# Kernel tuning notes

Measured on AMD Instinct MI355X. Metric: run time of the kernel, lower is better.

Reference implementation:

```python
import jax, jax.numpy as jnp
import numpy as np

G = 20000   # total_genes = nodes per graph = output dim
HID = 64    # hidden_channels
H = 4       # attention heads (concat=False -> mean over heads)
E = 640000  # edges (avg degree 32)
B = 128     # batch of cell-line samples
PD = 600    # perturbation feature dim
NEG_SLOPE = 0.2


def _gat(x, edge_index, W, a_src, a_dst, b, heads):
    """PyG GATConv with add_self_loops=True, concat=False (head mean)."""
    N = x.shape[0]
    C = W.shape[1] // heads
    h = (x @ W).reshape(N, heads, C)              # [N,H,C]
    loop = jnp.arange(N, dtype=edge_index.dtype)
    src = jnp.concatenate([edge_index[0], loop])  # [E+N]
    dst = jnp.concatenate([edge_index[1], loop])
    e_src = jnp.sum(h * a_src[None], axis=-1)     # [N,H]
    e_dst = jnp.sum(h * a_dst[None], axis=-1)
    e = jax.nn.leaky_relu(e_src[src] + e_dst[dst], NEG_SLOPE)  # [E+N,H]
    # segment softmax over incoming edges of each target node
    m = jax.ops.segment_max(e, dst, num_segments=N)
    ex = jnp.exp(e - m[dst])
    denom = jax.ops.segment_sum(ex, dst, num_segments=N)
    alpha = ex / denom[dst]                        # [E+N,H]
    out = jax.ops.segment_sum(h[src] * alpha[:, :, None], dst, num_segments=N)
    return out.mean(axis=1) + b                    # concat=False -> mean heads


def _mlp(x, W1, b1, W2, b2):
    # MLP([a,b,c], 'Sigmoid'): Linear -> Sigmoid -> Linear (last act dropped)
    return jax.nn.sigmoid(x @ W1 + b1) @ W2 + b2


def setup_inputs() -> dict:
    key = jax.random.key(0)
    ks = jax.random.split(key, 26)
    s = 0.05  # small init to keep sigmoids in their active range
    rn = lambda k, shp: jax.random.normal(k, shp, jnp.float32)
    return {
        "x": rn(ks[0], (G, 1)),
        "edge_index": jax.random.randint(ks[1], (2, E), 0, G, dtype=jnp.int32),
        "pos": jnp.arange(G, dtype=jnp.int32),
        "ctrl": rn(ks[2], (B, G)),
        "pert": rn(ks[3], (B, PD)),
        "gene_embed": rn(ks[4], (G, HID)) * s,
        "conv1_W": rn(ks[5], (1 + HID, H * HID)) * s,
        "conv1_as": rn(ks[6], (H, HID)) * s,
        "conv1_ad": rn(ks[7], (H, HID)) * s,
        "conv1_b": rn(ks[8], (HID,)) * s,
        "lin1_W": rn(ks[9], (1 + HID, HID)) * s,
        "lin1_b": rn(ks[10], (HID,)) * s,
        "conv2_W": rn(ks[11], (HID, H * 1)) * s,
        "conv2_as": rn(ks[12], (H, 1)) * s,
        "conv2_ad": rn(ks[13], (H, 1)) * s,
        "conv2_b": rn(ks[14], (1,)) * s,
        "lin2_W": rn(ks[15], (HID, 1)) * s,
        "lin2_b": rn(ks[16], (1,)) * s,
        "pert_W1": rn(ks[17], (PD, 128)) * s,
        "pert_b1": rn(ks[18], (128,)) * s,
        "pert_W2": rn(ks[19], (128, HID)) * s,
        "pert_b2": rn(ks[20], (HID,)) * s,
        "pred_W1": rn(ks[21], (G + HID, 1024)) * s,
        "pred_b1": rn(ks[22], (1024,)) * s,
        "pred_W2": rn(ks[23], (1024, G)) * s,
        "pred_b2": rn(ks[24], (G,)) * s,
    }


def reference(x, edge_index, pos, ctrl, pert, gene_embed,
              conv1_W, conv1_as, conv1_ad, conv1_b, lin1_W, lin1_b,
              conv2_W, conv2_as, conv2_ad, conv2_b, lin2_W, lin2_b,
              pert_W1, pert_b1, pert_W2, pert_b2,
              pred_W1, pred_b1, pred_W2, pred_b2):
    # per-graph GNN (single cell-type key), all_feat=True
    xc = jnp.concatenate([x, gene_embed[pos]], axis=1)         # [G, 1+HID]
    h1 = jax.nn.sigmoid(_gat(xc, edge_index, conv1_W, conv1_as, conv1_ad, conv1_b, H)
                        + xc @ lin1_W + lin1_b)                # [G, HID]
    h2 = jax.nn.sigmoid(_gat(h1, edge_index, conv2_W, conv2_as, conv2_ad, conv2_b, H)
                        + h1 @ lin2_W + lin2_b)                # [G, 1]
    feat = h2[:, 0]                                            # dense batch squeeze -> [G]
    # every sample in the batch uses this cell type's features
    z = feat[None, :] + ctrl                                   # [B, G]
    p = _mlp(pert, pert_W1, pert_b1, pert_W2, pert_b2)         # embd_pert -> [B, HID]
    inp = jnp.concatenate([z, p], axis=1)                      # [B, G+HID]
    return _mlp(inp, pred_W1, pred_b1, pred_W2, pred_b2)       # [B, G]
```

## Files before the change

### kernel.cpp

```cpp
#include <hip/hip_runtime.h>
#include <math.h>

#define G 20000
#define E_EDGES 640000
#define HID 64
#define NHEAD 4
#define BATCH 128
#define PD 600
#define NEG 0.2f
#define MAXE 256

#define KA1 20096
#define NSTEP1 628
#define KSPLIT1 32
#define KA2 1024

#define ROWS_HC 16

typedef float v4f __attribute__((ext_vector_type(4)));
typedef short short8 __attribute__((ext_vector_type(8)));

__device__ __forceinline__ float sigmoidf_(float x){ return 1.0f/(1.0f+__expf(-x)); }
__device__ __forceinline__ float leakyf_(float x){ return x>=0.f ? x : NEG*x; }
__device__ __forceinline__ unsigned short f2bf(float f){
    unsigned int u = __float_as_uint(f);
    return (unsigned short)((u + 0x7FFFu + ((u >> 16) & 1u)) >> 16);
}
__device__ __forceinline__ float bf2f(unsigned short b){
    return __uint_as_float(((unsigned int)b) << 16);
}

__global__ __launch_bounds__(320)
void k_hc(const float* __restrict__ x, const int* __restrict__ pos,
          const float* __restrict__ ge, const float* __restrict__ Wc,
          const float* __restrict__ Wl, const float* __restrict__ as_,
          const float* __restrict__ ad_,
          unsigned short* __restrict__ hcb, float* __restrict__ hlin,
          float* __restrict__ es, float* __restrict__ ed)
{
    int t = threadIdx.x;
    int rb = blockIdx.x * ROWS_HC;
    __shared__ float xc[ROWS_HC][68];
    for (int l = t; l < ROWS_HC*65; l += 320){
        int r = l / 65, k = l - r*65;
        int row = rb + r;
        float v = 0.f;
        if (row < G) v = (k == 0) ? x[row] : ge[pos[row]*HID + (k-1)];
        xc[r][k] = v;
    }
    float wcol[65];
    if (t < 256){
        #pragma unroll
        for (int k = 0; k < 65; ++k) wcol[k] = Wc[k*256 + t];
    } else {
        int c = t - 256;
        #pragma unroll
        for (int k = 0; k < 65; ++k) wcol[k] = Wl[k*64 + c];
    }
    float a_s = 0.f, a_d = 0.f;
    if (t < 256){ a_s = as_[t]; a_d = ad_[t]; }
    __syncthreads();

    int nrow = G - rb; if (nrow > ROWS_HC) nrow = ROWS_HC;
    for (int r = 0; r < nrow; ++r){
        int row = rb + r;
        const float4* xr = (const float4*)&xc[r][0];
        float acc = 0.f;
        #pragma unroll
        for (int k4 = 0; k4 < 16; ++k4){
            float4 v = xr[k4];
            acc += v.x*wcol[4*k4] + v.y*wcol[4*k4+1] + v.z*wcol[4*k4+2] + v.w*wcol[4*k4+3];
        }
        acc += xc[r][64] * wcol[64];
        if (t < 256){
            hcb[(size_t)row*256 + t] = f2bf(acc);
            float v1 = acc * a_s, v2 = acc * a_d;
            #pragma unroll
            for (int m = 32; m; m >>= 1){ v1 += __shfl_xor(v1, m); v2 += __shfl_xor(v2, m); }
            if ((t & 63) == 0){ int h = t >> 6; es[row*4+h] = v1; ed[row*4+h] = v2; }
        } else {
            hlin[(size_t)row*64 + (t - 256)] = acc;
        }
    }
}

__global__ void k_hist(const int* __restrict__ ei, int* __restrict__ cnt){
    int e = blockIdx.x*blockDim.x + threadIdx.x;
    if (e < E_EDGES) atomicAdd(&cnt[ei[E_EDGES + e]], 1);
}
__global__ void k_scan(const int* __restrict__ cnt, int* __restrict__ offs,
                       int* __restrict__ cur)
{
    __shared__ int ts[1024];
    int t = threadIdx.x;
    int base = t * 20;
    int loc[20];
    int s = 0;
    #pragma unroll
    for (int j = 0; j < 20; ++j){
        int i = base + j;
        int v = (i < G) ? cnt[i] : 0;
        loc[j] = s; s += v;
    }
    ts[t] = s;
    __syncthreads();
    for (int off = 1; off < 1024; off <<= 1){
        int add = (t >= off) ? ts[t - off] : 0;
        __syncthreads();
        ts[t] += add;
        __syncthreads();
    }
    int tb = (t == 0) ? 0 : ts[t - 1];
    #pragma unroll
    for (int j = 0; j < 20; ++j){
        int i = base + j;
        if (i < G){ int o = tb + loc[j]; offs[i] = o; cur[i] = o; }
    }
    if (t == 0) offs[G] = ts[1023];
}
__global__ void k_scatter(const int* __restrict__ ei, int* __restrict__ cur, int* __restrict__ csr){
    int e = blockIdx.x*blockDim.x + threadIdx.x;
    if (e < E_EDGES){
        int d = ei[E_EDGES + e];
        int p = atomicAdd(&cur[d], 1);
        csr[p] = ei[e];
    }
}

__global__ __launch_bounds__(256)
void k_gat1(const unsigned short* __restrict__ hcb, const float* __restrict__ hlin,
            const float* __restrict__ es, const float* __restrict__ ed,
            const int* __restrict__ offs, const int* __restrict__ csr,
            const float* __restrict__ bc1, const float* __restrict__ bl1,
            float* __restrict__ h1)
{
    int d = blockIdx.x; int t = threadIdx.x;
    int lane = t & 63, wv = t >> 6;
    __shared__ float4 cache[MAXE];
    __shared__ int    ssrc[MAXE];
    __shared__ float  wredm[4][4];
    __shared__ float  wreds[4][4];
    __shared__ float  red[256];
    int o = offs[d];
    int deg = offs[d+1] - o;
    int total = deg + 1;
    if (total > MAXE) total = MAXE;
    float4 edv = *(const float4*)(ed + d*4);
    float mx0=-1e30f, mx1=-1e30f, mx2=-1e30f, mx3=-1e30f;
    for (int idx = t; idx < total; idx += 256){
        int s = (idx < deg) ? csr[o + idx] : d;
        ssrc[idx] = s;
        float4 ev = *(const float4*)(es + s*4);
        float e0 = leakyf_(ev.x + edv.x);
        float e1 = leakyf_(ev.y + edv.y);
        float e2 = leakyf_(ev.z + edv.z);
        float e3 = leakyf_(ev.w + edv.w);
        cache[idx] = make_float4(e0, e1, e2, e3);
        mx0 = fmaxf(mx0, e0); mx1 = fmaxf(mx1, e1);
        mx2 = fmaxf(mx2, e2); mx3 = fmaxf(mx3, e3);
    }
    #pragma unroll
    for (int m = 32; m; m >>= 1){
        mx0 = fmaxf(mx0, __shfl_xor(mx0, m)); mx1 = fmaxf(mx1, __shfl_xor(mx1, m));
        mx2 = fmaxf(mx2, __shfl_xor(mx2, m)); mx3 = fmaxf(mx3, __shfl_xor(mx3, m));
    }
    if (lane == 0){ wredm[wv][0]=mx0; wredm[wv][1]=mx1; wredm[wv][2]=mx2; wredm[wv][3]=mx3; }
    __syncthreads();
    float m0 = fmaxf(fmaxf(wredm[0][0], wredm[1][0]), fmaxf(wredm[2][0], wredm[3][0]));
    float m1 = fmaxf(fmaxf(wredm[0][1], wredm[1][1]), fmaxf(wredm[2][1], wredm[3][1]));
    float m2 = fmaxf(fmaxf(wredm[0][2], wredm[1][2]), fmaxf(wredm[2][2], wredm[3][2]));
    float m3 = fmaxf(fmaxf(wredm[0][3], wredm[1][3]), fmaxf(wredm[2][3], wredm[3][3]));
    float s0=0.f, s1=0.f, s2=0.f, s3=0.f;
    for (int idx = t; idx < total; idx += 256){
        float4 cv = cache[idx];
        float e0 = __expf(cv.x - m0);
        float e1 = __expf(cv.y - m1);
        float e2 = __expf(cv.z - m2);
        float e3 = __expf(cv.w - m3);
        cache[idx] = make_float4(e0, e1, e2, e3);
        s0 += e0; s1 += e1; s2 += e2; s3 += e3;
    }
    #pragma unroll
    for (int m = 32; m; m >>= 1){
        s0 += __shfl_xor(s0, m); s1 += __shfl_xor(s1, m);
        s2 += __shfl_xor(s2, m); s3 += __shfl_xor(s3, m);
    }
    if (lane == 0){ wreds[wv][0]=s0; wreds[wv][1]=s1; wreds[wv][2]=s2; wreds[wv][3]=s3; }
    __syncthreads();
    float inv = 1.0f / (wreds[0][wv] + wreds[1][wv] + wreds[2][wv] + wreds[3][wv]);
    float acc0 = 0.f, acc1 = 0.f;
    int idx = 0;
    for (; idx + 2 <= total; idx += 2){
        int sA = ssrc[idx], sB = ssrc[idx+1];
        float aA = ((const float*)&cache[idx])[wv];
        float aB = ((const float*)&cache[idx+1])[wv];
        acc0 += aA * bf2f(hcb[(size_t)sA*256 + t]);
        acc1 += aB * bf2f(hcb[(size_t)sB*256 + t]);
    }
    if (idx < total){
        acc0 += ((const float*)&cache[idx])[wv] * bf2f(hcb[(size_t)ssrc[idx]*256 + t]);
    }
    red[t] = (acc0 + acc1) * inv;
    __syncthreads();
    if (t < 64){
        float sum = red[t] + red[64+t] + red[128+t] + red[192+t];
        float val = 0.25f*sum + bc1[t] + hlin[(size_t)d*64 + t] + bl1[t];
        h1[d*64 + t] = sigmoidf_(val);
    }
}

__global__ void k_conv2prep(const float* __restrict__ h1, const float* __restrict__ W2c,
                            const float* __restrict__ as2, const float* __restrict__ ad2,
                            const float* __restrict__ Wl2, float* __restrict__ hh2,
                            float* __restrict__ es2, float* __restrict__ ed2,
                            float* __restrict__ lv)
{
    int i = blockIdx.x; int k = threadIdx.x;
    float hv = h1[i*64 + k];
    #pragma unroll
    for (int j = 0; j < 4; ++j){
        float v = hv * W2c[k*4 + j];
        for (int m = 32; m; m >>= 1) v += __shfl_xor(v, m);
        if (k == 0){ hh2[i*4+j] = v; es2[i*4+j] = v*as2[j]; ed2[i*4+j] = v*ad2[j]; }
    }
    float v = hv * Wl2[k];
    for (int m = 32; m; m >>= 1) v += __shfl_xor(v, m);
    if (k == 0) lv[i] = v;
}

__global__ void k_gat2(const float* __restrict__ hh2, const float* __restrict__ es2,
                       const float* __restrict__ ed2, const int* __restrict__ offs,
                       const int* __restrict__ csr, const float* __restrict__ lv,
                       const float* __restrict__ bc2, const float* __restrict__ bl2,
                       float* __restrict__ feat)
{
    int d = blockIdx.x; int j = threadIdx.x;
    int o = offs[d];
    int deg = offs[d+1] - o;
    int total = deg + 1;
    float edst[4];
    #pragma unroll
    for (int h = 0; h < 4; ++h) edst[h] = ed2[d*4+h];
    float lmax[4] = {-1e30f,-1e30f,-1e30f,-1e30f};
    for (int idx = j; idx < total; idx += 64){
        int s = (idx < deg) ? csr[o + idx] : d;
        #pragma unroll
        for (int h = 0; h < 4; ++h)
            lmax[h] = fmaxf(lmax[h], leakyf_(es2[s*4+h] + edst[h]));
    }
    #pragma unroll
    for (int h = 0; h < 4; ++h)
        for (int m = 32; m; m >>= 1) lmax[h] = fmaxf(lmax[h], __shfl_xor(lmax[h], m));
    float lsum[4] = {0.f,0.f,0.f,0.f};
    float lnum[4] = {0.f,0.f,0.f,0.f};
    for (int idx = j; idx < total; idx += 64){
        int s = (idx < deg) ? csr[o + idx] : d;
        #pragma unroll
        for (int h = 0; h < 4; ++h){
            float e  = leakyf_(es2[s*4+h] + edst[h]);
            float ex = __expf(e - lmax[h]);
            lsum[h] += ex;
            lnum[h] += ex * hh2[s*4+h];
        }
    }
    #pragma unroll
    for (int h = 0; h < 4; ++h){
        for (int m = 32; m; m >>= 1){ lsum[h] += __shfl_xor(lsum[h], m); lnum[h] += __shfl_xor(lnum[h], m); }
    }
    if (j == 0){
        float sum = 0.f;
        #pragma unroll
        for (int h = 0; h < 4; ++h) sum += lnum[h] / lsum[h];
        feat[d] = sigmoidf_(0.25f*sum + bc2[0] + lv[d] + bl2[0]);
    }
}

__global__ void k_prepA(const float* __restrict__ ctrl, const float* __restrict__ feat,
                        unsigned short* __restrict__ Abf)
{
    int col = blockIdx.x*256 + threadIdx.x;
    int row = blockIdx.y;
    if (col < 20000)
        Abf[(size_t)row*KA1 + col] = f2bf(ctrl[(size_t)row*20000 + col] + feat[col]);
}

__global__ void k_pert(const float* __restrict__ pert, const float* __restrict__ W1,
                       const float* __restrict__ b1, const float* __restrict__ W2,
                       const float* __restrict__ b2, unsigned short* __restrict__ Abf)
{
    int r = blockIdx.x; int t = threadIdx.x;
    __shared__ float hid[128];
    float acc = 0.f;
    for (int k = 0; k < PD; ++k) acc += pert[r*PD + k] * W1[k*128 + t];
    hid[t] = sigmoidf_(acc + b1[t]);
    __syncthreads();
    if (t < 64){
        float a2 = 0.f;
        for (int k = 0; k < 128; ++k) a2 += hid[k] * W2[k*64 + t];
        Abf[(size_t)r*KA1 + 20000 + t] = f2bf(a2 + b2[t]);
    } else if (t < 96){
        Abf[(size_t)r*KA1 + 20000 + t] = 0;
    }
}

__global__ __launch_bounds__(256, 2)
void k_gemm1m(const unsigned short* __restrict__ Abf, const float* __restrict__ W1,
              float* __restrict__ part)
{
    int t = threadIdx.x;
    int lane = t & 63, wv = t >> 6;
    int lane16 = lane & 15, quad = lane >> 4, quad8 = quad * 8;
    int colbase = blockIdx.x * 64;
    int ks = blockIdx.y;
    int sbeg = (ks * NSTEP1) / KSPLIT1;
    int send = ((ks + 1) * NSTEP1) / KSPLIT1;
    int nsteps = send - sbeg;
    int kbeg = sbeg * 32;
    __shared__ unsigned short Bs[2][32*64];

    v4f acc[8];
    #pragma unroll
    for (int i = 0; i < 8; ++i) acc[i] = (v4f){0.f,0.f,0.f,0.f};

    int krow = t >> 3;
    int ng   = (t & 7) * 8;
    {
        int kg = kbeg + krow;
        short8 p;
        if (kg < 20064){
            float4 a = *(const float4*)(W1 + (size_t)kg*1024 + colbase + ng);
            float4 b = *(const float4*)(W1 + (size_t)kg*1024 + colbase + ng + 4);
            p[0]=(short)f2bf(a.x); p[1]=(short)f2bf(a.y); p[2]=(short)f2bf(a.z); p[3]=(short)f2bf(a.w);
            p[4]=(short)f2bf(b.x); p[5]=(short)f2bf(b.y); p[6]=(short)f2bf(b.z); p[7]=(short)f2bf(b.w);
        } else {
            p = (short8){0,0,0,0,0,0,0,0};
        }
        *(short8*)&Bs[0][krow*64 + ng] = p;
    }
    __syncthreads();

    int cur = 0;
    for (int s = 0; s < nsteps; ++s){
        int kg = kbeg + s*32;
        short8 bfrag;
        #pragma unroll
        for (int j = 0; j < 8; ++j)
            bfrag[j] = (short)Bs[cur][(quad8 + j)*64 + wv*16 + lane16];
        float w[8];
        bool more = (s + 1) < nsteps;
        if (more){
            int kn = kg + 32 + krow;
            if (kn < 20064){
                float4 a = *(const float4*)(W1 + (size_t)kn*1024 + colbase + ng);
                float4 b = *(const float4*)(W1 + (size_t)kn*1024 + colbase + ng + 4);
                w[0]=a.x; w[1]=a.y; w[2]=a.z; w[3]=a.w; w[4]=b.x; w[5]=b.y; w[6]=b.z; w[7]=b.w;
            } else {
                #pragma unroll
                for (int i = 0; i < 8; ++i) w[i] = 0.f;
            }
        }
        #pragma unroll
        for (int mt = 0; mt < 8; ++mt){
            short8 af = *(const short8*)(Abf + (size_t)(mt*16 + lane16)*KA1 + kg + quad8);
            acc[mt] = __builtin_amdgcn_mfma_f32_16x16x32_bf16(af, bfrag, acc[mt], 0, 0, 0);
        }
        if (more){
            short8 p;
            #pragma unroll
            for (int i = 0; i < 8; ++i) p[i] = (short)f2bf(w[i]);
            *(short8*)&Bs[cur^1][krow*64 + ng] = p;
        }
        __syncthreads();
        cur ^= 1;
    }
    float* dst = part + (size_t)ks * 131072;
    int col = colbase + wv*16 + lane16;
    #pragma unroll
    for (int mt = 0; mt < 8; ++mt)
        #pragma unroll
        for (int r = 0; r < 4; ++r)
            dst[(size_t)(mt*16 + quad*4 + r)*1024 + col] = acc[mt][r];
}

__global__ void k_reduce(const float* __restrict__ part, const float* __restrict__ b1,
                         unsigned short* __restrict__ hidbf)
{
    int row = blockIdx.x;
    int col = blockIdx.y*256 + threadIdx.x;
    float s = 0.f;
    #pragma unroll
    for (int ks = 0; ks < KSPLIT1; ++ks)
        s += part[(size_t)ks*131072 + (size_t)row*1024 + col];
    hidbf[(size_t)row*1024 + col] = f2bf(sigmoidf_(s + b1[col]));
}

__global__ __launch_bounds__(256, 2)
void k_gemm2m(const unsigned short* __restrict__ hidbf, const float* __restrict__ W2,
              const float* __restrict__ b2, float* __restrict__ out)
{
    int t = threadIdx.x;
    int lane = t & 63, wv = t >> 6;
    int lane16 = lane & 15, quad = lane >> 4, quad8 = quad * 8;
    int colbase = blockIdx.x * 64;
    int rbase   = blockIdx.y * 64;
    __shared__ unsigned short Bs[2][32*64];

    v4f acc[4];
    #pragma unroll
    for (int i = 0; i < 4; ++i) acc[i] = (v4f){0.f,0.f,0.f,0.f};

    int krow = t >> 3;
    int ng   = (t & 7) * 8;
    bool cv = (colbase + ng) < 20000;
    {
        short8 p = (short8){0,0,0,0,0,0,0,0};
        if (cv){
            float4 a = *(const float4*)(W2 + (size_t)krow*20000 + colbase + ng);
            float4 b = *(const float4*)(W2 + (size_t)krow*20000 + colbase + ng + 4);
            p[0]=(short)f2bf(a.x); p[1]=(short)f2bf(a.y); p[2]=(short)f2bf(a.z); p[3]=(short)f2bf(a.w);
            p[4]=(short)f2bf(b.x); p[5]=(short)f2bf(b.y); p[6]=(short)f2bf(b.z); p[7]=(short)f2bf(b.w);
        }
        *(short8*)&Bs[0][krow*64 + ng] = p;
    }
    __syncthreads();

    int cur = 0;
    for (int s = 0; s < 32; ++s){
        int kg = s*32;
        short8 bfrag;
        #pragma unroll
        for (int j = 0; j < 8; ++j)
            bfrag[j] = (short)Bs[cur][(quad8 + j)*64 + wv*16 + lane16];
        float w[8];
        bool more = s < 31;
        if (more){
            if (cv){
                int kn = kg + 32 + krow;
                float4 a = *(const float4*)(W2 + (size_t)kn*20000 + colbase + ng);
                float4 b = *(const float4*)(W2 + (size_t)kn*20000 + colbase + ng + 4);
                w[0]=a.x; w[1]=a.y; w[2]=a.z; w[3]=a.w; w[4]=b.x; w[5]=b.y; w[6]=b.z; w[7]=b.w;
            } else {
                #pragma unroll
                for (int i = 0; i < 8; ++i) w[i] = 0.f;
            }
        }
        #pragma unroll
        for (int mt = 0; mt < 4; ++mt){
            short8 af = *(const short8*)(hidbf + (size_t)(rbase + mt*16 + lane16)*KA2 + kg + quad8);
            acc[mt] = __builtin_amdgcn_mfma_f32_16x16x32_bf16(af, bfrag, acc[mt], 0, 0, 0);
        }
        if (more){
            short8 p;
            #pragma unroll
            for (int i = 0; i < 8; ++i) p[i] = (short)f2bf(w[i]);
            *(short8*)&Bs[cur^1][krow*64 + ng] = p;
        }
        __syncthreads();
        cur ^= 1;
    }
    int col = colbase + wv*16 + lane16;
    if (col < 20000){
        float bb = b2[col];
        #pragma unroll
        for (int mt = 0; mt < 4; ++mt)
            #pragma unroll
            for (int r = 0; r < 4; ++r)
                out[(size_t)(rbase + mt*16 + quad*4 + r)*20000 + col] = acc[mt][r] + bb;
    }
}

extern "C" void kernel_launch(void* const* d_in, const int* in_sizes, int n_in,
                              void* d_out, int out_size, void* d_ws, size_t ws_size,
                              hipStream_t stream)
{
    const float* x    = (const float*)d_in[0];
    const int*   ei   = (const int*)  d_in[1];
    const int*   pos  = (const int*)  d_in[2];
    const float* ctrl = (const float*)d_in[3];
    const float* pert = (const float*)d_in[4];
    const float* ge   = (const float*)d_in[5];
    const float* c1W  = (const float*)d_in[6];
    const float* c1as = (const float*)d_in[7];
    const float* c1ad = (const float*)d_in[8];
    const float* c1b  = (const float*)d_in[9];
    const float* l1W  = (const float*)d_in[10];
    const float* l1b  = (const float*)d_in[11];
    const float* c2W  = (const float*)d_in[12];
    const float* c2as = (const float*)d_in[13];
    const float* c2ad = (const float*)d_in[14];
    const float* c2b  = (const float*)d_in[15];
    const float* l2W  = (const float*)d_in[16];
    const float* l2b  = (const float*)d_in[17];
    const float* pW1  = (const float*)d_in[18];
    const float* pb1  = (const float*)d_in[19];
    const float* pW2  = (const float*)d_in[20];
    const float* pb2  = (const float*)d_in[21];
    const float* prW1 = (const float*)d_in[22];
    const float* prb1 = (const float*)d_in[23];
    const float* prW2 = (const float*)d_in[24];
    const float* prb2 = (const float*)d_in[25];
    float* out = (float*)d_out;

    char* ws = (char*)d_ws;
    size_t off = 0;
    auto alloc = [&](size_t bytes)->void*{
        void* pp = ws + off;
        off += (bytes + 255) & ~(size_t)255;
        return pp;
    };
    unsigned short* hcb  = (unsigned short*)alloc((size_t)G*256*2);
    float* hlin = (float*)alloc((size_t)G*64*4);
    float* h1   = (float*)alloc((size_t)G*64*4);
    float* es1  = (float*)alloc((size_t)G*4*4);
    float* ed1  = (float*)alloc((size_t)G*4*4);
    float* hh2  = (float*)alloc((size_t)G*4*4);
    float* es2  = (float*)alloc((size_t)G*4*4);
    float* ed2  = (float*)alloc((size_t)G*4*4);
    float* lv   = (float*)alloc((size_t)G*4);
    float* feat = (float*)alloc((size_t)G*4);
    unsigned short* hidbf = (unsigned short*)alloc((size_t)128*KA2*2);
    unsigned short* Abf1  = (unsigned short*)alloc((size_t)128*KA1*2);
    float* part = (float*)alloc((size_t)KSPLIT1*131072*4);
    int*   cnt  = (int*)alloc((size_t)G*4);
    int*   offs = (int*)alloc((size_t)(G+1)*4);
    int*   cur  = (int*)alloc((size_t)G*4);
    int*   csr  = (int*)alloc((size_t)E_EDGES*4);

    hipMemsetAsync(cnt, 0, (size_t)G*4, stream);

    k_hist   <<<(E_EDGES+255)/256, 256, 0, stream>>>(ei, cnt);
    k_scan   <<<1, 1024, 0, stream>>>(cnt, offs, cur);
    k_scatter<<<(E_EDGES+255)/256, 256, 0, stream>>>(ei, cur, csr);

    k_hc       <<<(G + ROWS_HC - 1)/ROWS_HC, 320, 0, stream>>>(x, pos, ge, c1W, l1W, c1as, c1ad,
                                         hcb, hlin, es1, ed1);
    k_gat1     <<<G, 256, 0, stream>>>(hcb, hlin, es1, ed1, offs, csr, c1b, l1b, h1);
    k_conv2prep<<<G, 64, 0, stream>>>(h1, c2W, c2as, c2ad, l2W, hh2, es2, ed2, lv);
    k_gat2     <<<G, 64, 0, stream>>>(hh2, es2, ed2, offs, csr, lv, c2b, l2b, feat);

    dim3 gp(79, 128);
    k_prepA<<<gp, 256, 0, stream>>>(ctrl, feat, Abf1);
    k_pert <<<BATCH, 128, 0, stream>>>(pert, pW1, pb1, pW2, pb2, Abf1);

    dim3 g1(16, KSPLIT1);
    k_gemm1m<<<g1, 256, 0, stream>>>(Abf1, prW1, part);
    dim3 gr(128, 4);
    k_reduce<<<gr, 256, 0, stream>>>(part, prb1, hidbf);
    dim3 g2(313, 2);
    k_gemm2m<<<g2, 256, 0, stream>>>(hidbf, prW2, prb2, out);
}
```

Baseline: 647.3 us.

## Split GAT1 aggregation across waves by edge with vectorized bf16 row loads

Reworks the attention-weighted aggregation in the first GAT kernel. Each of the four waves now takes every fourth edge and reads a full 256-element bf16 row with 8-byte vector loads, where before each wave handled one head and walked every edge with 2-byte loads. The next edge's row is prefetched one iteration ahead. A cross-wave shared-memory reduction then regathers the per-head, per-feature sums. The aim is fewer, wider memory transactions per gathered row, paid for with a more complex final reduction that has strided LDS reads.

```diff
diff --git a/kernel.cpp b/kernel.cpp
--- a/kernel.cpp
+++ b/kernel.cpp
@@ -140,7 +140,7 @@
     __shared__ int    ssrc[MAXE];
     __shared__ float  wredm[4][4];
     __shared__ float  wreds[4][4];
-    __shared__ float  red[256];
+    __shared__ float4 red[256];
     int o = offs[d];
     int deg = offs[d+1] - o;
     int total = deg + 1;
@@ -187,23 +187,44 @@
     }
     if (lane == 0){ wreds[wv][0]=s0; wreds[wv][1]=s1; wreds[wv][2]=s2; wreds[wv][3]=s3; }
     __syncthreads();
-    float inv = 1.0f / (wreds[0][wv] + wreds[1][wv] + wreds[2][wv] + wreds[3][wv]);
-    float acc0 = 0.f, acc1 = 0.f;
-    int idx = 0;
-    for (; idx + 2 <= total; idx += 2){
-        int sA = ssrc[idx], sB = ssrc[idx+1];
-        float aA = ((const float*)&cache[idx])[wv];
-        float aB = ((const float*)&cache[idx+1])[wv];
-        acc0 += aA * bf2f(hcb[(size_t)sA*256 + t]);
-        acc1 += aB * bf2f(hcb[(size_t)sB*256 + t]);
-    }
-    if (idx < total){
-        acc0 += ((const float*)&cache[idx])[wv] * bf2f(hcb[(size_t)ssrc[idx]*256 + t]);
-    }
-    red[t] = (acc0 + acc1) * inv;
+
+    int u = lane;
+    int h = u >> 4;
+    float inv = 1.0f / (wreds[0][h] + wreds[1][h] + wreds[2][h] + wreds[3][h]);
+    float a0=0.f, a1=0.f, a2=0.f, a3=0.f;
+    uint2 v; float al;
+    bool act = (wv < total);
+    if (act){
+        int s = ssrc[wv];
+        al = ((const float*)&cache[wv])[h];
+        v = *(const uint2*)(hcb + (size_t)s*256 + u*4);
+    }
+    for (int base = wv; base < total; ){
+        uint2 vc = v; float ac = al;
+        int nb = base + 4;
+        if (nb < total){
+            int s2 = ssrc[nb];
+            al = ((const float*)&cache[nb])[h];
+            v = *(const uint2*)(hcb + (size_t)s2*256 + u*4);
+        }
+        a0 += ac * __uint_as_float(vc.x << 16);
+        a1 += ac * __uint_as_float(vc.x & 0xFFFF0000u);
+        a2 += ac * __uint_as_float(vc.y << 16);
+        a3 += ac * __uint_as_float(vc.y & 0xFFFF0000u);
+        base = nb;
+    }
+    red[t] = make_float4(a0*inv, a1*inv, a2*inv, a3*inv);
     __syncthreads();
     if (t < 64){
-        float sum = red[t] + red[64+t] + red[128+t] + red[192+t];
+        float sum = 0.f;
+        #pragma unroll
+        for (int hh = 0; hh < 4; ++hh){
+            int f = hh*64 + t;
+            int uu = f >> 2, slot = f & 3;
+            #pragma unroll
+            for (int g = 0; g < 4; ++g)
+                sum += ((const float*)&red[g*64 + uu])[slot];
+        }
         float val = 0.25f*sum + bc1[t] + hlin[(size_t)d*64 + t] + bl1[t];
         h1[d*64 + t] = sigmoidf_(val);
     }
```

After: 618.7 us. -4.4%, faster.
